# Optimization experiments

Hardware: AMD Instinct MI355X
Metric: run time of the kernel (lower is better)

Reference implementation:

```python
import jax, jax.numpy as jnp
import numpy as np

B, T, S, L_SRC, V, H, E, AV = 16, 128, 192, 192, 30522, 768, 768, 200
L_ORG = L_SRC - 1
KEEP, DEL, STOP, PAD = 3, 4, 2, 0  # SP_IDS = [KEEP, DEL, INSERT, STOP, PAD, LEFT, RIGHT, MARK]


def lstm(x, Wih, Whh, bih, bhh):
    # x: [B, T, E] -> outputs [B, T, H]; PyTorch gate order i, f, g, o
    Bx = x.shape[0]
    Hh = Whh.shape[1]
    def step(carry, xt):
        h, c = carry
        g = xt @ Wih.T + bih + h @ Whh.T + bhh
        i, f, gg, o = jnp.split(g, 4, axis=-1)
        c = jax.nn.sigmoid(f) * c + jax.nn.sigmoid(i) * jnp.tanh(gg)
        h = jax.nn.sigmoid(o) * jnp.tanh(c)
        return (h, c), h
    h0 = jnp.zeros((Bx, Hh), x.dtype)
    _, hs = jax.lax.scan(step, (h0, h0), jnp.swapaxes(x, 0, 1))
    return jnp.swapaxes(hs, 0, 1)


def compute_counters(input_edits, org_ids):
    # Vectorized replica of the host-side numpy counter bookkeeping.
    # Emits the PRE-update counters used at each timestep t (updated with gold = input_edits[:, t+1]).
    Bx = input_edits.shape[0]
    golds = jnp.swapaxes(input_edits[:, 1:], 0, 1)  # [T-1, B]
    barange = jnp.arange(Bx)
    Lorg = org_ids.shape[1]
    def step(carry, g):
        cd, ci, ca = carry
        pre = (cd, ci, ca)
        cd2 = cd + ((g == KEEP) | (g == DEL)).astype(jnp.int32)
        alive = (g != DEL) & (g != STOP) & (g != PAD)
        ci2 = ci + alive.astype(jnp.int32)
        nxt = jnp.clip(ca + 1, 0, Lorg - 1)
        tok = org_ids[barange, nxt]
        cond = alive & (g != KEEP) & (ca + 1 < Lorg) & ((tok == 103) | (tok == 3) | (tok == 4))
        ca2 = jnp.where(cond, ca + 1, jnp.maximum(cd2, ca))
        return (cd2, ci2, ca2), pre
    z = jnp.zeros((Bx,), jnp.int32)
    _, (cds, cis, cas) = jax.lax.scan(step, (z, z, z), golds)
    return jnp.swapaxes(cds, 0, 1), jnp.swapaxes(cis, 0, 1), jnp.swapaxes(cas, 0, 1)  # each [B, T-1]


def setup_inputs():
    key = jax.random.key(0)
    ks = jax.random.split(key, 40)
    s = 0.02
    rn = lambda k, sh: jax.random.normal(k, sh, jnp.float32) * s
    inp = {
        "input_edits": jax.random.randint(ks[0], (B, T), 0, 12),
        "input_actions": jax.random.randint(ks[1], (B, T), 0, AV),
        "simp_sent": jax.random.randint(ks[2], (B, S), 0, V),
        "org_ids": jax.random.randint(ks[3], (B, L_ORG), 0, V),
        "encoder_outputs_org": jax.random.normal(ks[4], (B, L_SRC, H), jnp.float32),
        "emb": rn(ks[5], (V, E)),
    }
    i = 6
    for nm in ("e", "a", "w"):
        inp["Wih_" + nm] = rn(ks[i], (4 * H, E)); i += 1
        inp["Whh_" + nm] = rn(ks[i], (4 * H, H)); i += 1
        inp["bih_" + nm] = jnp.zeros((4 * H,), jnp.float32)
        inp["bhh_" + nm] = jnp.zeros((4 * H,), jnp.float32)
    inp["W_align"] = rn(ks[i], (H, H)); i += 1
    inp["W_proj"] = rn(ks[i], (H, H)); i += 1
    inp["W_ref"] = rn(ks[i], (2, H)); i += 1
    inp["b_ref"] = jnp.zeros((2,), jnp.float32)
    inp["W_mlp"] = rn(ks[i], (E, 5 * H)); i += 1
    inp["b_mlp"] = jnp.zeros((E,), jnp.float32)
    inp["W_act"] = rn(ks[i], (E, 5 * H)); i += 1
    inp["b_act"] = jnp.zeros((E,), jnp.float32)
    inp["W_out"] = rn(ks[i], (V, E)); i += 1
    inp["b_out"] = jnp.zeros((V,), jnp.float32)
    inp["W_outact"] = rn(ks[i], (AV, E)); i += 1
    inp["b_outact"] = jnp.zeros((AV,), jnp.float32)
    m = np.full((1, AV), -100000.0, dtype=np.float32)
    m[0, [0, 1, 2, 5, 101, 102]] = 0.0
    inp["action_mask"] = jnp.asarray(m)
    return inp


def reference(input_edits, input_actions, simp_sent, org_ids, encoder_outputs_org, emb,
              Wih_e, Whh_e, bih_e, bhh_e, Wih_a, Whh_a, bih_a, bhh_a, Wih_w, Whh_w, bih_w, bhh_w,
              W_align, W_proj, W_ref, b_ref, W_mlp, b_mlp, W_act, b_act,
              W_out, b_out, W_outact, b_outact, action_mask):
    # tanh(output_hidden_alignment(enc)) then drop the first (CLS) position
    enc = jnp.tanh(encoder_outputs_org @ W_align.T)[:, 1:]  # [B, L_ORG, H]
    out_e = lstm(emb[input_edits], Wih_e, Whh_e, bih_e, bhh_e)
    out_a = lstm(emb[input_actions], Wih_a, Whh_a, bih_a, bhh_a)
    out_w = lstm(emb[simp_sent], Wih_w, Whh_w, bih_w, bhh_w)
    cd, ci, ca = compute_counters(input_edits, org_ids)  # [B, T-1] each
    Tm1 = input_edits.shape[1] - 1
    bidx = jnp.arange(enc.shape[0])[:, None]
    c_input = enc[bidx, cd]   # [B, T-1, H] data-dependent gather per timestep
    c_anno = enc[bidx, ca]
    c_word = out_w[bidx, ci]
    dec_e = out_e[:, :Tm1]
    dec_a = out_a[:, :Tm1]
    c_pair = jnp.stack([c_input, c_anno], axis=2)  # [B, T-1, 2, H]
    wref_e = jax.nn.softmax(dec_e @ W_ref.T + b_ref, axis=-1)
    wref_a = jax.nn.softmax(dec_a @ W_ref.T + b_ref, axis=-1)
    c_edit = jnp.einsum('btk,btkh->bth', wref_e, c_pair)
    c_action = jnp.einsum('btk,btkh->bth', wref_a, c_pair)
    attn = jax.nn.softmax(jnp.einsum('bth,blh->btl', c_word @ W_proj.T, enc), axis=-1)
    applied = jnp.einsum('btl,blh->bth', attn, enc)
    feat_a = jnp.concatenate([dec_a, dec_e, applied, c_action, c_word], axis=-1)
    act_log = jax.nn.log_softmax(jnp.tanh(feat_a @ W_act.T + b_act) @ W_outact.T + b_outact + action_mask[0], axis=-1)
    feat_e = jnp.concatenate([dec_e, dec_a, applied, c_edit, c_word], axis=-1)
    edit_log = jax.nn.log_softmax(jnp.tanh(feat_e @ W_mlp.T + b_mlp) @ W_out.T + b_out, axis=-1)
    return edit_log, act_log
```

## Files before the change

### kernel.cpp

```cpp
#include <hip/hip_runtime.h>
#include <hip/hip_bf16.h>

typedef __hip_bfloat16 bf16;

#define B_    16
#define T_    128
#define S_    192
#define H_    768
#define G4_   3072
#define V_    30522
#define AV_   200
#define L_    191
#define TM1_  127
#define R_    2032
#define K5_   3840
#define NB_   48
#define HSL_  16

typedef short bf16x8_t __attribute__((ext_vector_type(8)));
typedef float f32x4_t  __attribute__((ext_vector_type(4)));

__device__ __forceinline__ float bf2f(bf16 v) { return __bfloat162float(v); }
__device__ __forceinline__ bf16  f2bf(float v) { return __float2bfloat16(v); }
__device__ __forceinline__ unsigned short f2us(float v) { bf16 h = f2bf(v); return *reinterpret_cast<unsigned short*>(&h); }
__device__ __forceinline__ float uslo(unsigned u) { union { unsigned i; float f; } x; x.i = u << 16; return x.f; }
__device__ __forceinline__ float ushi(unsigned u) { union { unsigned i; float f; } x; x.i = u & 0xffff0000u; return x.f; }
__device__ __forceinline__ float us2f(unsigned short u) { union { unsigned i; float f; } x; x.i = ((unsigned)u) << 16; return x.f; }
__device__ __forceinline__ float sigm(float x) { return 1.0f / (1.0f + expf(-x)); }

__device__ __forceinline__ bf16x8_t ld8bf(const bf16* p) { return *(const bf16x8_t*)p; }
__device__ __forceinline__ bf16x8_t ld8bf(const float* p) {
    float4 a = *(const float4*)p;
    float4 b = *(const float4*)(p + 4);
    bf16x8_t r;
    r[0] = (short)f2us(a.x); r[1] = (short)f2us(a.y); r[2] = (short)f2us(a.z); r[3] = (short)f2us(a.w);
    r[4] = (short)f2us(b.x); r[5] = (short)f2us(b.y); r[6] = (short)f2us(b.z); r[7] = (short)f2us(b.w);
    return r;
}

template <typename TA, typename TW>
__global__ __launch_bounds__(256) void gemm_mfma(
    const TA* __restrict__ A, const TW* __restrict__ W,
    const float* __restrict__ bias1, const float* __restrict__ bias2,
    bf16* __restrict__ Ch, float* __restrict__ Cf,
    int M, int N, int K, int act, int rowdiv, int lda)
{
    __shared__ short As[128][40];
    __shared__ short Ws[128][40];
    const int tid = threadIdx.x;
    const int wave = tid >> 6, lane = tid & 63;
    const int mw = (wave >> 1) * 64, nw = (wave & 1) * 64;
    const int bm = blockIdx.x * 128, bn = blockIdx.y * 128;

    const int sr = tid >> 2;
    const int sc = (tid & 3) * 8;

    f32x4_t acc[4][4];
#pragma unroll
    for (int mi = 0; mi < 4; ++mi)
#pragma unroll
        for (int ni = 0; ni < 4; ++ni) acc[mi][ni] = (f32x4_t){0.f, 0.f, 0.f, 0.f};

    const int fr = lane & 15;
    const int fk = (lane >> 4) * 8;

    for (int k0 = 0; k0 < K; k0 += 32) {
#pragma unroll
        for (int c = 0; c < 2; ++c) {
            const int row = sr + c * 64;
            int ga = bm + row; if (ga > M - 1) ga = M - 1;
            const int ra = (rowdiv > 0) ? (ga + ga / rowdiv + 1) : ga;
            *(bf16x8_t*)&As[row][sc] = ld8bf(A + (size_t)ra * lda + k0 + sc);
            int gw = bn + row; if (gw > N - 1) gw = N - 1;
            *(bf16x8_t*)&Ws[row][sc] = ld8bf(W + (size_t)gw * K + k0 + sc);
        }
        __syncthreads();
        bf16x8_t af[4], wf[4];
#pragma unroll
        for (int i = 0; i < 4; ++i) af[i] = *(const bf16x8_t*)&As[mw + i * 16 + fr][fk];
#pragma unroll
        for (int i = 0; i < 4; ++i) wf[i] = *(const bf16x8_t*)&Ws[nw + i * 16 + fr][fk];
#pragma unroll
        for (int mi = 0; mi < 4; ++mi)
#pragma unroll
            for (int ni = 0; ni < 4; ++ni)
                acc[mi][ni] = __builtin_amdgcn_mfma_f32_16x16x32_bf16(af[mi], wf[ni], acc[mi][ni], 0, 0, 0);
        __syncthreads();
    }

    const int cl = lane & 15;
    const int rg = (lane >> 4) * 4;
#pragma unroll
    for (int mi = 0; mi < 4; ++mi) {
#pragma unroll
        for (int ni = 0; ni < 4; ++ni) {
            const int col = bn + nw + ni * 16 + cl;
            if (col >= N) continue;
#pragma unroll
            for (int j = 0; j < 4; ++j) {
                const int row = bm + mw + mi * 16 + rg + j;
                if (row >= M) continue;
                float v = acc[mi][ni][j];
                if (bias1) v += bias1[col];
                if (bias2) v += bias2[col];
                if (act == 1) v = tanhf(v);
                if (Ch) Ch[(size_t)row * N + col] = f2bf(v);
                else    Cf[(size_t)row * N + col] = v;
            }
        }
    }
}

__global__ void f2b_kernel(const float* __restrict__ in, bf16* __restrict__ out, int n4)
{
    const int i = blockIdx.x * 256 + threadIdx.x;
    if (i >= n4) return;
    float4 v = *(const float4*)(in + (size_t)i * 4);
    ushort4 o;
    o.x = f2us(v.x); o.y = f2us(v.y); o.z = f2us(v.z); o.w = f2us(v.w);
    *(ushort4*)(out + (size_t)i * 4) = o;
}

__global__ __launch_bounds__(256) void lstm_mfma_kernel(
    const bf16* __restrict__ pxe, const bf16* __restrict__ pxa, const bf16* __restrict__ pxw,
    const float* __restrict__ We, const float* __restrict__ Wa, const float* __restrict__ Ww,
    bf16* __restrict__ oute, bf16* __restrict__ outa, bf16* __restrict__ outw,
    unsigned short* __restrict__ hbuf, int* __restrict__ flags)
{
    const int which = blockIdx.x / NB_;
    const int nb = blockIdx.x % NB_;
    const bf16* px; const float* W; bf16* out; int Tn;
    if (which == 0)      { px = pxe; W = We; out = oute; Tn = T_; }
    else if (which == 1) { px = pxa; W = Wa; out = outa; Tn = T_; }
    else                 { px = pxw; W = Ww; out = outw; Tn = S_; }
    unsigned short* hG = hbuf + (size_t)which * (2 * B_ * H_);
    int* flg = flags + which * 64;

    const int tid = threadIdx.x;
    const int wv = tid >> 6;
    const int lane = tid & 63;
    const int so = nb * HSL_;

    __shared__ unsigned short hL[16][776];
    __shared__ float gS[4][16][17];
    __shared__ unsigned short oring[8][16][16];

    bf16x8_t Afrag[24];
    {
        const int m = lane & 15;
        const int kb8 = (lane >> 4) * 8;
        const float* wrow = W + (size_t)(wv * H_ + so + m) * H_ + kb8;
#pragma unroll
        for (int kb = 0; kb < 24; ++kb) {
            float4 f0 = *(const float4*)(wrow + kb * 32);
            float4 f1 = *(const float4*)(wrow + kb * 32 + 4);
            bf16x8_t a;
            a[0] = (short)f2us(f0.x); a[1] = (short)f2us(f0.y);
            a[2] = (short)f2us(f0.z); a[3] = (short)f2us(f0.w);
            a[4] = (short)f2us(f1.x); a[5] = (short)f2us(f1.y);
            a[6] = (short)f2us(f1.z); a[7] = (short)f2us(f1.w);
            Afrag[kb] = a;
        }
    }

    for (int i = tid; i < 16 * 776; i += 256) ((unsigned short*)hL)[i] = 0;

    const int cb = tid >> 4;
    const int chl = tid & 15;
    float c = 0.f;

    const int bn = lane & 15;
    const int bk = (lane >> 4) * 8;

    unsigned short pxr0, pxr1, pxr2, pxr3;
    {
        const bf16* q = px + ((size_t)cb * Tn + 0) * G4_ + so + chl;
        pxr0 = *(const unsigned short*)(q);
        pxr1 = *(const unsigned short*)(q + H_);
        pxr2 = *(const unsigned short*)(q + 2 * H_);
        pxr3 = *(const unsigned short*)(q + 3 * H_);
    }

    int cur = 0;
    for (int step = 0; step < Tn; ++step) {
        if (step > 0) {
            const unsigned long long* hsrc =
                (const unsigned long long*)(hG + (size_t)cur * (B_ * H_));
            for (int i = tid; i < B_ * H_ / 4; i += 256) {
                const unsigned long long v =
                    __hip_atomic_load(hsrc + i, __ATOMIC_RELAXED, __HIP_MEMORY_SCOPE_AGENT);
                const int bb = i / (H_ / 4);
                const int cc = i - bb * (H_ / 4);
                ((unsigned long long*)&hL[bb][0])[cc] = v;
            }
        }
        __syncthreads();

        f32x4_t acc = {0.f, 0.f, 0.f, 0.f};
#pragma unroll
        for (int kb = 0; kb < 24; ++kb) {
            bf16x8_t bfr = *(const bf16x8_t*)&hL[bn][kb * 32 + bk];
            acc = __builtin_amdgcn_mfma_f32_16x16x32_bf16(Afrag[kb], bfr, acc, 0, 0, 0);
        }
        {
            const int m0 = (lane >> 4) * 4;
#pragma unroll
            for (int j = 0; j < 4; ++j) gS[wv][m0 + j][bn] = acc[j];
        }
        __syncthreads();

        {
            const float gi = gS[0][chl][cb] + us2f(pxr0);
            const float gf = gS[1][chl][cb] + us2f(pxr1);
            const float gg = gS[2][chl][cb] + us2f(pxr2);
            const float go = gS[3][chl][cb] + us2f(pxr3);
            const float cn = sigm(gf) * c + sigm(gi) * tanhf(gg);
            const float hn = sigm(go) * tanhf(cn);
            c = cn;
            oring[step & 7][cb][chl] = f2us(hn);
            __hip_atomic_store(&hG[(size_t)(cur ^ 1) * (B_ * H_) + cb * H_ + so + chl],
                               f2us(hn), __ATOMIC_RELAXED, __HIP_MEMORY_SCOPE_AGENT);
        }
        if ((step & 7) == 7 || step == Tn - 1) {
            const int base = step & ~7;
            const int cnt8 = (step & 7) + 1;
            for (int s2 = 0; s2 < cnt8; ++s2)
                out[((size_t)cb * Tn + base + s2) * H_ + so + chl] =
                    *reinterpret_cast<const bf16*>(&oring[s2][cb][chl]);
        }

        if (step + 1 < Tn) {
            __syncthreads();
            const int target = step + 1;
            if (tid == 0)
                __hip_atomic_store(&flg[nb], target, __ATOMIC_RELAXED, __HIP_MEMORY_SCOPE_AGENT);
            {
                const bf16* q = px + ((size_t)cb * Tn + target) * G4_ + so + chl;
                pxr0 = *(const unsigned short*)(q);
                pxr1 = *(const unsigned short*)(q + H_);
                pxr2 = *(const unsigned short*)(q + 2 * H_);
                pxr3 = *(const unsigned short*)(q + 3 * H_);
            }
            if (lane < NB_) {
                long guard = 0;
                while (__hip_atomic_load(&flg[lane], __ATOMIC_RELAXED, __HIP_MEMORY_SCOPE_AGENT) < target) {
                    __builtin_amdgcn_s_sleep(1);
                    if (++guard > 50000000L) break;
                }
            }
        }
        cur ^= 1;
    }
}

__global__ void gather_rows_kernel(const int* __restrict__ ids,
                                   const float* __restrict__ emb,
                                   bf16* __restrict__ out)
{
    const int r = blockIdx.x;
    const float4* src = (const float4*)(emb + (size_t)ids[r] * H_);
    ushort4* dst = (ushort4*)(out + (size_t)r * H_);
    for (int h = threadIdx.x; h < H_ / 4; h += 256) {
        float4 v = src[h];
        ushort4 o;
        o.x = f2us(v.x); o.y = f2us(v.y); o.z = f2us(v.z); o.w = f2us(v.w);
        dst[h] = o;
    }
}

__global__ void counters_kernel(const int* __restrict__ edits, const int* __restrict__ org,
                                int* __restrict__ cd, int* __restrict__ ci, int* __restrict__ ca)
{
    const int b = threadIdx.x;
    if (b >= B_) return;
    int vd = 0, vi = 0, va = 0;
    for (int t = 0; t < TM1_; ++t) {
        cd[b * TM1_ + t] = vd; ci[b * TM1_ + t] = vi; ca[b * TM1_ + t] = va;
        const int g = edits[b * T_ + t + 1];
        const int vd2 = vd + ((g == 3 || g == 4) ? 1 : 0);
        const int alive = (g != 4 && g != 2 && g != 0) ? 1 : 0;
        const int vi2 = vi + alive;
        int nxt = va + 1; if (nxt > L_ - 1) nxt = L_ - 1;
        const int tok = org[b * L_ + nxt];
        const bool cond = alive && (g != 3) && (va + 1 < L_) && (tok == 103 || tok == 3 || tok == 4);
        const int va2 = cond ? (va + 1) : max(vd2, va);
        vd = vd2; vi = vi2; va = va2;
    }
}

__global__ void gather_cword_kernel(const bf16* __restrict__ outw, const int* __restrict__ ci,
                                    bf16* __restrict__ cw)
{
    const int r = blockIdx.x;
    const int b = r / TM1_;
    const unsigned* src = (const unsigned*)(outw + ((size_t)b * S_ + ci[r]) * H_);
    unsigned* dst = (unsigned*)(cw + (size_t)r * H_);
    for (int h = threadIdx.x; h < H_ / 2; h += 256) dst[h] = src[h];
}

__global__ __launch_bounds__(256) void ref_combine_kernel(
    const bf16* __restrict__ oute, const bf16* __restrict__ outa, const bf16* __restrict__ enc,
    const float* __restrict__ Wref, const float* __restrict__ bref,
    const int* __restrict__ cd, const int* __restrict__ ca,
    bf16* __restrict__ ced, bf16* __restrict__ cac)
{
    const int r = blockIdx.x;
    const int b = r / TM1_;
    const int t = r % TM1_;
    const bf16* de = oute + ((size_t)b * T_ + t) * H_;
    const bf16* da = outa + ((size_t)b * T_ + t) * H_;
    const int tid = threadIdx.x;
    __shared__ float red[256][4];
    float s0 = 0.f, s1 = 0.f, s2 = 0.f, s3 = 0.f;
    for (int k = tid; k < H_; k += 256) {
        const float w0 = Wref[k];
        const float w1 = Wref[H_ + k];
        const float e = bf2f(de[k]);
        const float a = bf2f(da[k]);
        s0 += e * w0; s1 += e * w1; s2 += a * w0; s3 += a * w1;
    }
    red[tid][0] = s0; red[tid][1] = s1; red[tid][2] = s2; red[tid][3] = s3;
    __syncthreads();
    for (int off = 128; off > 0; off >>= 1) {
        if (tid < off) {
            red[tid][0] += red[tid + off][0];
            red[tid][1] += red[tid + off][1];
            red[tid][2] += red[tid + off][2];
            red[tid][3] += red[tid + off][3];
        }
        __syncthreads();
    }
    const float br0 = bref[0], br1 = bref[1];
    const float xe0 = red[0][0] + br0, xe1 = red[0][1] + br1;
    const float xa0 = red[0][2] + br0, xa1 = red[0][3] + br1;
    const float me = fmaxf(xe0, xe1);
    const float ee0 = expf(xe0 - me), ee1 = expf(xe1 - me);
    const float pe0 = ee0 / (ee0 + ee1), pe1 = ee1 / (ee0 + ee1);
    const float ma = fmaxf(xa0, xa1);
    const float ea0 = expf(xa0 - ma), ea1 = expf(xa1 - ma);
    const float pa0 = ea0 / (ea0 + ea1), pa1 = ea1 / (ea0 + ea1);

    const bf16* ei = enc + ((size_t)b * L_ + cd[r]) * H_;
    const bf16* ea = enc + ((size_t)b * L_ + ca[r]) * H_;
    for (int h = tid; h < H_; h += 256) {
        const float vi = bf2f(ei[h]);
        const float va = bf2f(ea[h]);
        ced[(size_t)r * H_ + h] = f2bf(pe0 * vi + pe1 * va);
        cac[(size_t)r * H_ + h] = f2bf(pa0 * vi + pa1 * va);
    }
}

__global__ __launch_bounds__(256) void attn_kernel(const bf16* __restrict__ q,
                                                   const bf16* __restrict__ enc,
                                                   bf16* __restrict__ app)
{
    const int r = blockIdx.x;
    const int b = r / TM1_;
    const int tid = threadIdx.x;
    __shared__ float qs[H_];
    __shared__ float p[L_ + 1];
    __shared__ float red[256];
    const bf16* qrow = q + (size_t)r * H_;
    for (int h = tid; h < H_; h += 256) qs[h] = bf2f(qrow[h]);
    __syncthreads();
    const bf16* eb = enc + (size_t)b * L_ * H_;
    float myv = -1e30f;
    if (tid < L_) {
        const unsigned* er = (const unsigned*)(eb + (size_t)tid * H_);
        float s = 0.f;
        for (int k2 = 0; k2 < H_ / 2; ++k2) {
            const unsigned u = er[k2];
            s += qs[2 * k2] * uslo(u) + qs[2 * k2 + 1] * ushi(u);
        }
        p[tid] = s;
        myv = s;
    }
    red[tid] = myv;
    __syncthreads();
    for (int off = 128; off > 0; off >>= 1) {
        if (tid < off) red[tid] = fmaxf(red[tid], red[tid + off]);
        __syncthreads();
    }
    const float m = red[0];
    __syncthreads();
    float e = 0.f;
    if (tid < L_) e = expf(p[tid] - m);
    red[tid] = e;
    __syncthreads();
    for (int off = 128; off > 0; off >>= 1) {
        if (tid < off) red[tid] += red[tid + off];
        __syncthreads();
    }
    const float invZ = 1.f / red[0];
    __syncthreads();
    if (tid < L_) p[tid] = e * invZ;
    __syncthreads();
    for (int h = tid; h < H_; h += 256) {
        float s = 0.f;
        for (int l = 0; l < L_; ++l) s += p[l] * bf2f(eb[(size_t)l * H_ + h]);
        app[(size_t)r * H_ + h] = f2bf(s);
    }
}

__global__ void feat_kernel(const bf16* __restrict__ oute, const bf16* __restrict__ outa,
                            const bf16* __restrict__ app, const bf16* __restrict__ ced,
                            const bf16* __restrict__ cac, const bf16* __restrict__ cw,
                            bf16* __restrict__ fe, bf16* __restrict__ fa)
{
    const int r = blockIdx.x;
    const int b = r / TM1_;
    const int t = r % TM1_;
    const unsigned* de  = (const unsigned*)(oute + ((size_t)b * T_ + t) * H_);
    const unsigned* da  = (const unsigned*)(outa + ((size_t)b * T_ + t) * H_);
    const unsigned* ap  = (const unsigned*)(app + (size_t)r * H_);
    const unsigned* ce  = (const unsigned*)(ced + (size_t)r * H_);
    const unsigned* cA  = (const unsigned*)(cac + (size_t)r * H_);
    const unsigned* cwp = (const unsigned*)(cw + (size_t)r * H_);
    unsigned* pfe = (unsigned*)(fe + (size_t)r * K5_);
    unsigned* pfa = (unsigned*)(fa + (size_t)r * K5_);
    const int HW = H_ / 2;
    for (int h = threadIdx.x; h < HW; h += 256) {
        const unsigned ve = de[h], va = da[h], vap = ap[h], vce = ce[h], vca = cA[h], vcw = cwp[h];
        pfe[h] = ve;  pfe[HW + h] = va;  pfe[2 * HW + h] = vap; pfe[3 * HW + h] = vce; pfe[4 * HW + h] = vcw;
        pfa[h] = va;  pfa[HW + h] = ve;  pfa[2 * HW + h] = vap; pfa[3 * HW + h] = vca; pfa[4 * HW + h] = vcw;
    }
}

__global__ __launch_bounds__(1024) void logsoftmax_edit_kernel(float* __restrict__ out)
{
    float* row = out + (size_t)blockIdx.x * V_;
    const int tid = threadIdx.x;
    const int lane = tid & 63;
    const int wid = tid >> 6;
    __shared__ unsigned short rowb[V_];
    __shared__ float wredm[16], wreds[16];
    __shared__ float fin;

    float m = -1e30f, s = 0.f;
    for (int i = tid; i < V_; i += 1024) {
        const float x = row[i];
        rowb[i] = f2us(x);
        if (x > m) { s = s * expf(m - x) + 1.f; m = x; }
        else s += expf(x - m);
    }
#pragma unroll
    for (int off = 32; off > 0; off >>= 1) {
        const float m2 = __shfl_down(m, off);
        const float s2 = __shfl_down(s, off);
        const float mn = fmaxf(m, m2);
        s = s * expf(m - mn) + s2 * expf(m2 - mn);
        m = mn;
    }
    if (lane == 0) { wredm[wid] = m; wreds[wid] = s; }
    __syncthreads();
    if (wid == 0) {
        m = (lane < 16) ? wredm[lane] : -1e30f;
        s = (lane < 16) ? wreds[lane] : 0.f;
#pragma unroll
        for (int off = 8; off > 0; off >>= 1) {
            const float m2 = __shfl_down(m, off);
            const float s2 = __shfl_down(s, off);
            const float mn = fmaxf(m, m2);
            s = s * expf(m - mn) + s2 * expf(m2 - mn);
            m = mn;
        }
        if (lane == 0) fin = m + logf(s);
    }
    __syncthreads();
    const float lz = fin;
    for (int i = tid; i < V_; i += 1024) row[i] = us2f(rowb[i]) - lz;
}

__global__ __launch_bounds__(256) void logsoftmax_act_kernel(const float* __restrict__ in,
                                                             float* __restrict__ out)
{
    const float* row = in + (size_t)blockIdx.x * AV_;
    float* orow = out + (size_t)blockIdx.x * AV_;
    const int tid = threadIdx.x;
    __shared__ float red[256];
    float m = -1e30f;
    if (tid < AV_) m = row[tid];
    red[tid] = m;
    __syncthreads();
    for (int off = 128; off > 0; off >>= 1) {
        if (tid < off) red[tid] = fmaxf(red[tid], red[tid + off]);
        __syncthreads();
    }
    m = red[0];
    __syncthreads();
    float s = 0.f;
    if (tid < AV_) s = expf(row[tid] - m);
    red[tid] = s;
    __syncthreads();
    for (int off = 128; off > 0; off >>= 1) {
        if (tid < off) red[tid] += red[tid + off];
        __syncthreads();
    }
    const float lz = m + logf(red[0]);
    if (tid < AV_) orow[tid] = row[tid] - lz;
}

extern "C" void kernel_launch(void* const* d_in, const int* in_sizes, int n_in,
                              void* d_out, int out_size, void* d_ws, size_t ws_size,
                              hipStream_t stream)
{
    const int* input_edits   = (const int*)d_in[0];
    const int* input_actions = (const int*)d_in[1];
    const int* simp_sent     = (const int*)d_in[2];
    const int* org_ids       = (const int*)d_in[3];
    const float* enc_org     = (const float*)d_in[4];
    const float* emb         = (const float*)d_in[5];
    const float* Wih_e = (const float*)d_in[6];
    const float* Whh_e = (const float*)d_in[7];
    const float* bih_e = (const float*)d_in[8];
    const float* bhh_e = (const float*)d_in[9];
    const float* Wih_a = (const float*)d_in[10];
    const float* Whh_a = (const float*)d_in[11];
    const float* bih_a = (const float*)d_in[12];
    const float* bhh_a = (const float*)d_in[13];
    const float* Wih_w = (const float*)d_in[14];
    const float* Whh_w = (const float*)d_in[15];
    const float* bih_w = (const float*)d_in[16];
    const float* bhh_w = (const float*)d_in[17];
    const float* W_align = (const float*)d_in[18];
    const float* W_proj  = (const float*)d_in[19];
    const float* W_ref   = (const float*)d_in[20];
    const float* b_ref   = (const float*)d_in[21];
    const float* W_mlp   = (const float*)d_in[22];
    const float* b_mlp   = (const float*)d_in[23];
    const float* W_act   = (const float*)d_in[24];
    const float* b_act   = (const float*)d_in[25];
    const float* W_out   = (const float*)d_in[26];
    const float* b_out   = (const float*)d_in[27];
    const float* W_outact = (const float*)d_in[28];
    const float* b_outact = (const float*)d_in[29];
    const float* action_mask = (const float*)d_in[30];

    float* out = (float*)d_out;
    float* edit_out = out;
    float* act_out  = out + (size_t)R_ * V_;

    char* p = (char*)d_ws;
    auto take = [&](size_t bytes) { void* q = (void*)p; p += ((bytes + 255) / 256) * 256; return q; };
    int* flags = (int*)take(3 * 256);
    unsigned short* hbuf = (unsigned short*)take((size_t)3 * 2 * B_ * H_ * 2);
    char* alias_base = p;
    bf16* xe   = (bf16*)take((size_t)B_ * T_ * H_ * 2);
    bf16* xa   = (bf16*)take((size_t)B_ * T_ * H_ * 2);
    bf16* xw   = (bf16*)take((size_t)B_ * S_ * H_ * 2);
    bf16* pxe  = (bf16*)take((size_t)B_ * T_ * G4_ * 2);
    bf16* pxa  = (bf16*)take((size_t)B_ * T_ * G4_ * 2);
    bf16* pxw  = (bf16*)take((size_t)B_ * S_ * G4_ * 2);
    bf16* oute = (bf16*)take((size_t)B_ * T_ * H_ * 2);
    bf16* outa = (bf16*)take((size_t)B_ * T_ * H_ * 2);
    bf16* outw = (bf16*)take((size_t)B_ * S_ * H_ * 2);
    bf16* enc  = (bf16*)take((size_t)B_ * L_ * H_ * 2);
    bf16* cw   = (bf16*)take((size_t)R_ * H_ * 2);
    bf16* ced  = (bf16*)take((size_t)R_ * H_ * 2);
    bf16* cac  = (bf16*)take((size_t)R_ * H_ * 2);
    bf16* qb   = (bf16*)take((size_t)R_ * H_ * 2);
    bf16* app  = (bf16*)take((size_t)R_ * H_ * 2);
    bf16* fe   = (bf16*)take((size_t)R_ * K5_ * 2);
    bf16* fa   = (bf16*)take((size_t)R_ * K5_ * 2);
    bf16* he   = (bf16*)take((size_t)R_ * H_ * 2);
    bf16* ha   = (bf16*)take((size_t)R_ * H_ * 2);
    int*  cd   = (int*)take((size_t)R_ * 4);
    int*  ci   = (int*)take((size_t)R_ * 4);
    int*  ca   = (int*)take((size_t)R_ * 4);
    float* actbuf = (float*)take((size_t)R_ * AV_ * 4);
    bf16* Wob = (bf16*)alias_base;

    hipMemsetAsync(flags, 0, 3 * 256, stream);

    gather_rows_kernel<<<B_ * T_, 256, 0, stream>>>(input_edits, emb, xe);
    gather_rows_kernel<<<B_ * T_, 256, 0, stream>>>(input_actions, emb, xa);
    gather_rows_kernel<<<B_ * S_, 256, 0, stream>>>(simp_sent, emb, xw);

    dim3 gpx((B_ * T_ + 127) / 128, (G4_ + 127) / 128);
    gemm_mfma<bf16, float><<<gpx, 256, 0, stream>>>(xe, Wih_e, bih_e, bhh_e, pxe, nullptr, B_ * T_, G4_, H_, 0, 0, H_);
    gemm_mfma<bf16, float><<<gpx, 256, 0, stream>>>(xa, Wih_a, bih_a, bhh_a, pxa, nullptr, B_ * T_, G4_, H_, 0, 0, H_);
    dim3 gpxw((B_ * S_ + 127) / 128, (G4_ + 127) / 128);
    gemm_mfma<bf16, float><<<gpxw, 256, 0, stream>>>(xw, Wih_w, bih_w, bhh_w, pxw, nullptr, B_ * S_, G4_, H_, 0, 0, H_);

    dim3 genc((B_ * L_ + 127) / 128, (H_ + 127) / 128);
    gemm_mfma<float, float><<<genc, 256, 0, stream>>>(enc_org, W_align, nullptr, nullptr, enc, nullptr, B_ * L_, H_, H_, 1, L_, H_);

    counters_kernel<<<1, 64, 0, stream>>>(input_edits, org_ids, cd, ci, ca);

    lstm_mfma_kernel<<<3 * NB_, 256, 0, stream>>>(pxe, pxa, pxw, Whh_e, Whh_a, Whh_w,
                                                  oute, outa, outw, hbuf, flags);

    const int nW4 = V_ * H_ / 4;
    f2b_kernel<<<(nW4 + 255) / 256, 256, 0, stream>>>(W_out, Wob, nW4);

    gather_cword_kernel<<<R_, 256, 0, stream>>>(outw, ci, cw);

    ref_combine_kernel<<<R_, 256, 0, stream>>>(oute, outa, enc, W_ref, b_ref, cd, ca, ced, cac);

    dim3 gproj((R_ + 127) / 128, (H_ + 127) / 128);
    gemm_mfma<bf16, float><<<gproj, 256, 0, stream>>>(cw, W_proj, nullptr, nullptr, qb, nullptr, R_, H_, H_, 0, 0, H_);

    attn_kernel<<<R_, 256, 0, stream>>>(qb, enc, app);

    feat_kernel<<<R_, 256, 0, stream>>>(oute, outa, app, ced, cac, cw, fe, fa);

    gemm_mfma<bf16, float><<<gproj, 256, 0, stream>>>(fe, W_mlp, b_mlp, nullptr, he, nullptr, R_, H_, K5_, 1, 0, K5_);
    gemm_mfma<bf16, float><<<gproj, 256, 0, stream>>>(fa, W_act, b_act, nullptr, ha, nullptr, R_, H_, K5_, 1, 0, K5_);

    dim3 gact((R_ + 127) / 128, (AV_ + 127) / 128);
    gemm_mfma<bf16, float><<<gact, 256, 0, stream>>>(ha, W_outact, b_outact, action_mask, nullptr, actbuf, R_, AV_, H_, 0, 0, H_);
    logsoftmax_act_kernel<<<R_, 256, 0, stream>>>(actbuf, act_out);

    dim3 gedit((R_ + 127) / 128, (V_ + 127) / 128);
    gemm_mfma<bf16, bf16><<<gedit, 256, 0, stream>>>(he, Wob, b_out, nullptr, nullptr, edit_out, R_, V_, H_, 0, 0, H_);
    logsoftmax_edit_kernel<<<R_, 1024, 0, stream>>>(edit_out);
}
```

Before: 2.523 ms.

## Swizzle vocab GEMM block order and batch LSTM hidden-state publishing

The large vocab-projection GEMM now remaps its block indices so that the 8 blocks sharing a linear index modulo 8 cover adjacent N-tiles (likely one XCD each), with the grid padded to 240 columns and out-of-range blocks exiting early. This is meant to improve L2 reuse of the weight and activation tiles. In the LSTM, hidden-state publishing moves from per-thread 2-byte atomic stores to a single wave doing 8-byte stores from LDS, followed by a vmcnt wait before the flag is set. Output flushes are moved after the flag publish so they stay off the critical inter-block sync path. The cost is an extra syncthreads per step and reliance on the oring LDS layout for the vectorized copy.

```diff
diff --git a/kernel.cpp b/kernel.cpp
--- a/kernel.cpp
+++ b/kernel.cpp
@@ -43,14 +43,24 @@
     const TA* __restrict__ A, const TW* __restrict__ W,
     const float* __restrict__ bias1, const float* __restrict__ bias2,
     bf16* __restrict__ Ch, float* __restrict__ Cf,
-    int M, int N, int K, int act, int rowdiv, int lda)
+    int M, int N, int K, int act, int rowdiv, int lda, int swz)
 {
     __shared__ short As[128][40];
     __shared__ short Ws[128][40];
     const int tid = threadIdx.x;
     const int wave = tid >> 6, lane = tid & 63;
     const int mw = (wave >> 1) * 64, nw = (wave & 1) * 64;
-    const int bm = blockIdx.x * 128, bn = blockIdx.y * 128;
+
+    int bxi = blockIdx.x, byi = blockIdx.y;
+    if (swz > 0) {
+        const int lin = byi * gridDim.x + bxi;
+        const int x = lin & 7;
+        const int t = lin >> 3;
+        byi = x * swz + t / gridDim.x;
+        bxi = t % gridDim.x;
+        if (byi * 128 >= N) return;
+    }
+    const int bm = bxi * 128, bn = byi * 128;
 
     const int sr = tid >> 2;
     const int sc = (tid & 3) * 8;
@@ -218,28 +228,34 @@
             const float hn = sigm(go) * tanhf(cn);
             c = cn;
             oring[step & 7][cb][chl] = f2us(hn);
-            __hip_atomic_store(&hG[(size_t)(cur ^ 1) * (B_ * H_) + cb * H_ + so + chl],
-                               f2us(hn), __ATOMIC_RELAXED, __HIP_MEMORY_SCOPE_AGENT);
-        }
-        if ((step & 7) == 7 || step == Tn - 1) {
-            const int base = step & ~7;
-            const int cnt8 = (step & 7) + 1;
-            for (int s2 = 0; s2 < cnt8; ++s2)
-                out[((size_t)cb * Tn + base + s2) * H_ + so + chl] =
-                    *reinterpret_cast<const bf16*>(&oring[s2][cb][chl]);
-        }
+        }
+        __syncthreads();
 
         if (step + 1 < Tn) {
-            __syncthreads();
             const int target = step + 1;
-            if (tid == 0)
-                __hip_atomic_store(&flg[nb], target, __ATOMIC_RELAXED, __HIP_MEMORY_SCOPE_AGENT);
+            if (wv == 0) {
+                const int bb = lane >> 2, q = lane & 3;
+                const unsigned long long v =
+                    *(const unsigned long long*)&oring[step & 7][bb][q * 4];
+                __hip_atomic_store(
+                    (unsigned long long*)&hG[(size_t)(cur ^ 1) * (B_ * H_) + bb * H_ + so + q * 4],
+                    v, __ATOMIC_RELAXED, __HIP_MEMORY_SCOPE_AGENT);
+                asm volatile("s_waitcnt vmcnt(0)" ::: "memory");
+                if (tid == 0)
+                    __hip_atomic_store(&flg[nb], target, __ATOMIC_RELAXED, __HIP_MEMORY_SCOPE_AGENT);
+            }
             {
                 const bf16* q = px + ((size_t)cb * Tn + target) * G4_ + so + chl;
                 pxr0 = *(const unsigned short*)(q);
                 pxr1 = *(const unsigned short*)(q + H_);
                 pxr2 = *(const unsigned short*)(q + 2 * H_);
                 pxr3 = *(const unsigned short*)(q + 3 * H_);
+            }
+            if ((step & 7) == 7) {
+                const int base = step & ~7;
+                for (int s2 = 0; s2 < 8; ++s2)
+                    out[((size_t)cb * Tn + base + s2) * H_ + so + chl] =
+                        *reinterpret_cast<const bf16*>(&oring[s2][cb][chl]);
             }
             if (lane < NB_) {
                 long guard = 0;
@@ -248,6 +264,12 @@
                     if (++guard > 50000000L) break;
                 }
             }
+        } else {
+            const int base = step & ~7;
+            const int cnt8 = (step & 7) + 1;
+            for (int s2 = 0; s2 < cnt8; ++s2)
+                out[((size_t)cb * Tn + base + s2) * H_ + so + chl] =
+                    *reinterpret_cast<const bf16*>(&oring[s2][cb][chl]);
         }
         cur ^= 1;
     }
@@ -577,13 +599,13 @@
     gather_rows_kernel<<<B_ * S_, 256, 0, stream>>>(simp_sent, emb, xw);
 
     dim3 gpx((B_ * T_ + 127) / 128, (G4_ + 127) / 128);
-    gemm_mfma<bf16, float><<<gpx, 256, 0, stream>>>(xe, Wih_e, bih_e, bhh_e, pxe, nullptr, B_ * T_, G4_, H_, 0, 0, H_);
-    gemm_mfma<bf16, float><<<gpx, 256, 0, stream>>>(xa, Wih_a, bih_a, bhh_a, pxa, nullptr, B_ * T_, G4_, H_, 0, 0, H_);
+    gemm_mfma<bf16, float><<<gpx, 256, 0, stream>>>(xe, Wih_e, bih_e, bhh_e, pxe, nullptr, B_ * T_, G4_, H_, 0, 0, H_, 0);
+    gemm_mfma<bf16, float><<<gpx, 256, 0, stream>>>(xa, Wih_a, bih_a, bhh_a, pxa, nullptr, B_ * T_, G4_, H_, 0, 0, H_, 0);
     dim3 gpxw((B_ * S_ + 127) / 128, (G4_ + 127) / 128);
-    gemm_mfma<bf16, float><<<gpxw, 256, 0, stream>>>(xw, Wih_w, bih_w, bhh_w, pxw, nullptr, B_ * S_, G4_, H_, 0, 0, H_);
+    gemm_mfma<bf16, float><<<gpxw, 256, 0, stream>>>(xw, Wih_w, bih_w, bhh_w, pxw, nullptr, B_ * S_, G4_, H_, 0, 0, H_, 0);
 
     dim3 genc((B_ * L_ + 127) / 128, (H_ + 127) / 128);
-    gemm_mfma<float, float><<<genc, 256, 0, stream>>>(enc_org, W_align, nullptr, nullptr, enc, nullptr, B_ * L_, H_, H_, 1, L_, H_);
+    gemm_mfma<float, float><<<genc, 256, 0, stream>>>(enc_org, W_align, nullptr, nullptr, enc, nullptr, B_ * L_, H_, H_, 1, L_, H_, 0);
 
     counters_kernel<<<1, 64, 0, stream>>>(input_edits, org_ids, cd, ci, ca);
 
@@ -598,20 +620,20 @@
     ref_combine_kernel<<<R_, 256, 0, stream>>>(oute, outa, enc, W_ref, b_ref, cd, ca, ced, cac);
 
     dim3 gproj((R_ + 127) / 128, (H_ + 127) / 128);
-    gemm_mfma<bf16, float><<<gproj, 256, 0, stream>>>(cw, W_proj, nullptr, nullptr, qb, nullptr, R_, H_, H_, 0, 0, H_);
+    gemm_mfma<bf16, float><<<gproj, 256, 0, stream>>>(cw, W_proj, nullptr, nullptr, qb, nullptr, R_, H_, H_, 0, 0, H_, 0);
 
     attn_kernel<<<R_, 256, 0, stream>>>(qb, enc, app);
 
     feat_kernel<<<R_, 256, 0, stream>>>(oute, outa, app, ced, cac, cw, fe, fa);
 
-    gemm_mfma<bf16, float><<<gproj, 256, 0, stream>>>(fe, W_mlp, b_mlp, nullptr, he, nullptr, R_, H_, K5_, 1, 0, K5_);
-    gemm_mfma<bf16, float><<<gproj, 256, 0, stream>>>(fa, W_act, b_act, nullptr, ha, nullptr, R_, H_, K5_, 1, 0, K5_);
+    gemm_mfma<bf16, float><<<gproj, 256, 0, stream>>>(fe, W_mlp, b_mlp, nullptr, he, nullptr, R_, H_, K5_, 1, 0, K5_, 0);
+    gemm_mfma<bf16, float><<<gproj, 256, 0, stream>>>(fa, W_act, b_act, nullptr, ha, nullptr, R_, H_, K5_, 1, 0, K5_, 0);
 
     dim3 gact((R_ + 127) / 128, (AV_ + 127) / 128);
-    gemm_mfma<bf16, float><<<gact, 256, 0, stream>>>(ha, W_outact, b_outact, action_mask, nullptr, actbuf, R_, AV_, H_, 0, 0, H_);
+    gemm_mfma<bf16, float><<<gact, 256, 0, stream>>>(ha, W_outact, b_outact, action_mask, nullptr, actbuf, R_, AV_, H_, 0, 0, H_, 0);
     logsoftmax_act_kernel<<<R_, 256, 0, stream>>>(actbuf, act_out);
 
-    dim3 gedit((R_ + 127) / 128, (V_ + 127) / 128);
-    gemm_mfma<bf16, bf16><<<gedit, 256, 0, stream>>>(he, Wob, b_out, nullptr, nullptr, edit_out, R_, V_, H_, 0, 0, H_);
+    dim3 gedit(16, 240);
+    gemm_mfma<bf16, bf16><<<gedit, 256, 0, stream>>>(he, Wob, b_out, nullptr, nullptr, edit_out, R_, V_, H_, 0, 0, H_, 30);
     logsoftmax_edit_kernel<<<R_, 1024, 0, stream>>>(edit_out);
 }
```

New measurement: 2.690 ms. 6.6% more time.
